# Optimization experiments

Hardware: AMD Instinct MI355X
Metric: run time of the kernel (lower is better)

Reference implementation:

```python
import jax, jax.numpy as jnp
import numpy as np

B, D, M = 16384, 512, 16

def setup_inputs() -> dict:
    key = jax.random.key(0)
    k1, k2, k3 = jax.random.split(key, 3)
    z = jax.random.normal(k1, (B, D), dtype=jnp.float32)
    # Psi: n_dynamics small [D,D] operators (orthogonal-init in torch; random here)
    Psi = jax.random.normal(k2, (M, D, D), dtype=jnp.float32) * 0.001
    gate_tokens = jax.random.normal(k3, (M, D), dtype=jnp.float32) * (1.0 / np.sqrt(D))
    t = jnp.zeros((1,), dtype=jnp.float32)  # unused by forward, kept for signature parity
    return {"t": t, "z": z, "Psi": Psi, "gate_tokens": gate_tokens}

def reference(t, z, Psi, gate_tokens):
    # scores[b,m,e] = (z @ Psi_m)[b,e]  -- batched small GEMM over M dynamics
    scores = jnp.einsum('bd,mde->bme', z, Psi)
    # gate logits and sparse-soft gates: relu(2*sigmoid(logits) - 1)
    logits = jnp.einsum('bme,me->bm', scores, gate_tokens)
    gates = jax.nn.relu(2.0 * jax.nn.sigmoid(logits) - 1.0)
    # dz[b,e] = sum_m gates[b,m] * scores[b,m,e]
    dz = jnp.einsum('bm,bme->be', gates, scores)
    return dz
```

## Files before the change

### kernel.cpp

```cpp
#include <hip/hip_runtime.h>
#include <hip/hip_bf16.h>

#define B_N 16384
#define D_N 512
#define M_N 16

typedef __attribute__((ext_vector_type(4))) float  f32x4;
typedef __attribute__((ext_vector_type(8))) short  s16x8;

__device__ __forceinline__ short bf16_of(float f) {
  union { float f; unsigned u; } v; v.f = f;
  unsigned r = v.u + 0x7fffu + ((v.u >> 16) & 1u);
  return (short)(r >> 16);
}
__device__ __forceinline__ float f32_of_bf16(unsigned short u) {
  union { unsigned u; float f; } v; v.u = ((unsigned)u) << 16; return v.f;
}
__device__ __forceinline__ void gload_lds16(const void* g, void* l) {
  __builtin_amdgcn_global_load_lds(
      (const __attribute__((address_space(1))) unsigned*)g,
      (__attribute__((address_space(3))) unsigned*)l, 16, 0, 0);
}

#define MFMA_ACC(d, x, y) d = __builtin_amdgcn_mfma_f32_16x16x32_bf16(x, y, d, 0, 0, 0)
#define MFMA_Z(d, x, y)   d = __builtin_amdgcn_mfma_f32_16x16x32_bf16(x, y, FZERO, 0, 0, 0)

__global__ void k_trw(const float* __restrict__ Psi, const float* __restrict__ gt,
                      short* __restrict__ Psib, float* __restrict__ wT) {
  int m = blockIdx.y, d0 = blockIdx.x << 6;
  __shared__ float tile[64][65];
  __shared__ float gs[D_N];
  int t = threadIdx.x;
  for (int i = t; i < D_N; i += 256) gs[i] = gt[m * D_N + i];
  int r = t >> 2, q = t & 3;
  float wacc = 0.f;
  const float* src = Psi + (size_t)m * D_N * D_N;
  short* dst = Psib + (size_t)m * D_N * D_N;
  for (int e0 = 0; e0 < D_N; e0 += 64) {
    __syncthreads();
    #pragma unroll
    for (int j = 0; j < 4; ++j) {
      int idx = t + (j << 8);
      int rr = idx >> 4, c4 = idx & 15;
      *(f32x4*)&tile[rr][c4 * 4] = *(const f32x4*)(src + (size_t)(d0 + rr) * D_N + e0 + c4 * 4);
    }
    __syncthreads();
    #pragma unroll
    for (int k = 0; k < 16; ++k) wacc += tile[r][q * 16 + k] * gs[e0 + q * 16 + k];
    #pragma unroll
    for (int it = 0; it < 2; ++it) {
      int idx = t + (it << 8);
      int el = idx >> 3, jb = idx & 7;
      int e = e0 + el;
      s16x8 o;
      #pragma unroll
      for (int k = 0; k < 8; ++k) o[k] = bf16_of(tile[jb * 8 + k][el]);
      int db = jb ^ (e & 7);
      *(s16x8*)(dst + (size_t)e * D_N + d0 + db * 8) = o;
    }
  }
  wacc += __shfl_xor(wacc, 1);
  wacc += __shfl_xor(wacc, 2);
  if (q == 0) wT[(d0 + r) * M_N + m] = wacc;
}

__global__ void k_gz(const float* __restrict__ z, const float* __restrict__ wT,
                     short* __restrict__ zb, unsigned short* __restrict__ gatesb) {
  __shared__ float zs[16][D_N];
  int t = threadIdx.x;
  size_t b0 = (size_t)blockIdx.x * 16;
  #pragma unroll
  for (int j = 0; j < 8; ++j) {
    int idx = t + (j << 8);
    int r = idx >> 7, c4 = idx & 127;
    *(f32x4*)&zs[r][c4 * 4] = *(const f32x4*)(z + (b0 + r) * D_N + c4 * 4);
  }
  __syncthreads();
  int r = t >> 4, m = t & 15;
  float s0 = 0.f, s1 = 0.f, s2 = 0.f, s3 = 0.f;
  #pragma unroll 4
  for (int e = 0; e < D_N; e += 4) {
    s0 += zs[r][e + 0] * wT[(e + 0) * M_N + m];
    s1 += zs[r][e + 1] * wT[(e + 1) * M_N + m];
    s2 += zs[r][e + 2] * wT[(e + 2) * M_N + m];
    s3 += zs[r][e + 3] * wT[(e + 3) * M_N + m];
  }
  float s = (s0 + s1) + (s2 + s3);
  float sig = 1.f / (1.f + expf(-s));
  gatesb[(b0 + r) * M_N + m] = (unsigned short)bf16_of(fmaxf(2.f * sig - 1.f, 0.f));
  #pragma unroll
  for (int j = 0; j < 4; ++j) {
    int idx = t + (j << 8);
    int rr = idx >> 6, blk = idx & 63;
    int chunk = blk >> 3, ib = blk & 7;
    int sb = ib ^ (rr & 7);
    const float* sp = &zs[rr][chunk * 64 + sb * 8];
    s16x8 o;
    #pragma unroll
    for (int k = 0; k < 8; ++k) o[k] = bf16_of(sp[k]);
    *(s16x8*)(zb + (b0 + rr) * D_N + blk * 8) = o;
  }
}

__global__ __launch_bounds__(512, 2) void k_gemm(
    const char* __restrict__ zb, const unsigned short* __restrict__ gatesb,
    const char* __restrict__ pb, float* __restrict__ dz) {
  __shared__ __align__(128) char smem[147456];
  float* glf = (float*)(smem + 131072);

  const int tid = threadIdx.x;
  const int lane = tid & 63;
  const int wid = tid >> 6;
  const int wr = wid >> 1;
  const int wc = wid & 1;
  const int bid = blockIdx.x;
  const int xcd = bid & 7;
  const int g8 = bid >> 3;
  const int bcol = g8 & 3;
  const int brow = xcd * 8 + (g8 >> 2);

  {
    s16x8 gv = *(const s16x8*)(gatesb + ((size_t)brow << 12) + ((size_t)tid << 3));
    int row = tid >> 1, mbase = (tid & 1) << 3;
    #pragma unroll
    for (int k = 0; k < 8; ++k)
      glf[(mbase + k) * 256 + row] = f32_of_bf16((unsigned short)gv[k]);
  }

  const int rsub = lane >> 3, cbyte = (lane & 7) << 4;

  auto stageA = [&](int ab, int dc) {
    #pragma unroll
    for (int j = 0; j < 4; ++j) {
      const char* g = zb + (((size_t)(brow * 256 + wid * 8 + j * 64 + rsub)) << 10)
                      + (dc << 7) + cbyte;
      gload_lds16(g, smem + ab * 32768 + (wid << 10) + (j << 13));
    }
  };
  auto stageB = [&](int s) {
    int m = s & 15, dc = s >> 4, q = s & 3;
    #pragma unroll
    for (int j = 0; j < 2; ++j) {
      const char* g = pb + (((size_t)(m * 512 + bcol * 128 + wid * 8 + j * 64 + rsub)) << 10)
                      + (dc << 7) + cbyte;
      gload_lds16(g, smem + 65536 + q * 16384 + (wid << 10) + (j << 13));
    }
  };

  const int lrow = lane & 15;
  const int swz = (lrow & 7) << 4;
  const int kq16 = (((lane >> 4) << 4)) ^ swz;
  const int offY = ((wr * 64 + lrow) << 7) + kq16;
  const int offX = ((wc * 64 + lrow) << 7) + kq16;
  const int grow = wr * 64 + lrow;

  f32x4 acc[4][4] = {};
  f32x4 accm[4][4];
  s16x8 areg[4][2];
  s16x8 bx[4], by[4];
  float gjc[4], gjn[4];
  const f32x4 FZERO = {0.f, 0.f, 0.f, 0.f};

  stageA(0, 0);
  stageB(0); stageB(1); stageB(2);
  asm volatile("s_waitcnt vmcnt(0) lgkmcnt(0)" ::: "memory");
  __builtin_amdgcn_s_barrier();
  #pragma unroll
  for (int i = 0; i < 4; ++i)
    bx[i] = *(const s16x8*)(smem + 65536 + (offX + i * 2048));
  #pragma unroll
  for (int j = 0; j < 4; ++j)
    gjc[j] = glf[grow + j * 16];

  for (int s = 0; s < 128; ++s) {
    const int m = s & 15, dc = s >> 4;
    const char* bbase_cur = smem + 65536 + (s & 3) * 16384;
    const char* bbase_nxt = smem + 65536 + ((s + 1) & 3) * 16384;

    if (m == 0) {
      const char* abase = smem + (dc & 1) * 32768;
      #pragma unroll
      for (int j = 0; j < 4; ++j) {
        areg[j][0] = *(const s16x8*)(abase + (offY + j * 2048));
        areg[j][1] = *(const s16x8*)(abase + ((offY + j * 2048) ^ 64));
      }
    }
    #pragma unroll
    for (int i = 0; i < 4; ++i)
      by[i] = *(const s16x8*)(bbase_cur + ((offX + i * 2048) ^ 64));
    {
      const int mn = (s + 1) & 15;
      #pragma unroll
      for (int j = 0; j < 4; ++j)
        gjn[j] = glf[mn * 256 + grow + j * 16];
    }
    if (s + 3 < 128) stageB(s + 3);
    if (m == 11 && dc < 7) stageA((dc & 1) ^ 1, dc + 1);

    __builtin_amdgcn_s_setprio(1);
    #pragma unroll
    for (int i = 0; i < 4; ++i)
      #pragma unroll
      for (int j = 0; j < 4; ++j)
        MFMA_Z(accm[i][j], bx[i], areg[j][0]);
    __builtin_amdgcn_s_setprio(0);

    if (s < 127) {
      #pragma unroll
      for (int i = 0; i < 4; ++i)
        bx[i] = *(const s16x8*)(bbase_nxt + (offX + i * 2048));
    }

    __builtin_amdgcn_s_setprio(1);
    #pragma unroll
    for (int i = 0; i < 4; ++i)
      #pragma unroll
      for (int j = 0; j < 4; ++j)
        MFMA_ACC(accm[i][j], by[i], areg[j][1]);
    __builtin_amdgcn_s_setprio(0);
    #pragma unroll
    for (int i = 0; i < 4; ++i)
      #pragma unroll
      for (int j = 0; j < 4; ++j)
        #pragma unroll
        for (int jj = 0; jj < 4; ++jj)
          acc[i][j][jj] = fmaf(gjc[j], accm[i][j][jj], acc[i][j][jj]);
    #pragma unroll
    for (int j = 0; j < 4; ++j) gjc[j] = gjn[j];

    if (dc < 7 && (m == 11 || m == 12))
      asm volatile("s_waitcnt vmcnt(6)" ::: "memory");
    else if (s >= 125)
      asm volatile("s_waitcnt vmcnt(0)" ::: "memory");
    else
      asm volatile("s_waitcnt vmcnt(2)" ::: "memory");
    __builtin_amdgcn_s_barrier();
  }

  #pragma unroll
  for (int i = 0; i < 4; ++i) {
    int e = bcol * 128 + wc * 64 + i * 16 + ((lane >> 4) << 2);
    #pragma unroll
    for (int j = 0; j < 4; ++j) {
      size_t b = (size_t)brow * 256 + wr * 64 + j * 16 + lrow;
      *(f32x4*)(dz + b * D_N + e) = acc[i][j];
    }
  }
}

extern "C" void kernel_launch(void* const* d_in, const int* in_sizes, int n_in,
                              void* d_out, int out_size, void* d_ws, size_t ws_size,
                              hipStream_t stream) {
  const float* z   = (const float*)d_in[1];
  const float* Psi = (const float*)d_in[2];
  const float* gt  = (const float*)d_in[3];
  float* dz = (float*)d_out;

  float* wT = (float*)d_ws;
  unsigned short* gatesb = (unsigned short*)((char*)d_ws + 32768);
  short* Psib = (short*)((char*)d_ws + 32768 + 524288);
  short* zb16 = Psib + (size_t)M_N * D_N * D_N;

  k_trw <<<dim3(8, M_N), dim3(256), 0, stream>>>(Psi, gt, Psib, wT);
  k_gz  <<<dim3(B_N / 16), dim3(256), 0, stream>>>(z, wT, zb16, gatesb);
  k_gemm<<<dim3(256), dim3(512), 0, stream>>>((const char*)zb16, gatesb,
                                              (const char*)Psib, dz);
}
```

Before: 155.1 us.

## Split Psi transpose and gate-weight reduction into two more parallel kernels

The fused transpose-and-reduce kernel ran only 128 blocks, each walking all 512 columns serially. It is replaced by two kernels: one computing wT = Psi·gate_tokens with a wave per row (512 blocks), and one doing the bf16 transpose with a 3D grid of 1024 blocks, one 64x64 tile each. This raises parallelism in the preprocessing stage, at the cost of reading Psi twice and adding an extra launch.

```diff
diff --git a/kernel.cpp b/kernel.cpp
--- a/kernel.cpp
+++ b/kernel.cpp
@@ -25,43 +25,53 @@
 #define MFMA_ACC(d, x, y) d = __builtin_amdgcn_mfma_f32_16x16x32_bf16(x, y, d, 0, 0, 0)
 #define MFMA_Z(d, x, y)   d = __builtin_amdgcn_mfma_f32_16x16x32_bf16(x, y, FZERO, 0, 0, 0)
 
-__global__ void k_trw(const float* __restrict__ Psi, const float* __restrict__ gt,
-                      short* __restrict__ Psib, float* __restrict__ wT) {
-  int m = blockIdx.y, d0 = blockIdx.x << 6;
+__global__ void k_w(const float* __restrict__ Psi, const float* __restrict__ gt,
+                    float* __restrict__ wT) {
+  int m = blockIdx.x;
+  int d0 = blockIdx.y * 16;
+  __shared__ float g[D_N];
+  for (int i = threadIdx.x; i < D_N; i += 256) g[i] = gt[m * D_N + i];
+  __syncthreads();
+  int wave = threadIdx.x >> 6, lane = threadIdx.x & 63;
+  #pragma unroll
+  for (int d = d0 + wave; d < d0 + 16; d += 4) {
+    const float* row = Psi + ((size_t)m * D_N + d) * D_N;
+    const f32x4* r4 = (const f32x4*)(row + lane * 8);
+    const f32x4* g4 = (const f32x4*)(g + lane * 8);
+    f32x4 a0 = r4[0], a1 = r4[1];
+    f32x4 b0 = g4[0], b1 = g4[1];
+    float s = a0[0]*b0[0] + a0[1]*b0[1] + a0[2]*b0[2] + a0[3]*b0[3]
+            + a1[0]*b1[0] + a1[1]*b1[1] + a1[2]*b1[2] + a1[3]*b1[3];
+    #pragma unroll
+    for (int off = 32; off; off >>= 1) s += __shfl_down(s, off);
+    if (lane == 0) wT[d * M_N + m] = s;
+  }
+}
+
+__global__ void k_tr(const float* __restrict__ Psi, short* __restrict__ Psib) {
+  int m = blockIdx.z, d0 = blockIdx.x << 6, e0 = blockIdx.y << 6;
   __shared__ float tile[64][65];
-  __shared__ float gs[D_N];
   int t = threadIdx.x;
-  for (int i = t; i < D_N; i += 256) gs[i] = gt[m * D_N + i];
-  int r = t >> 2, q = t & 3;
-  float wacc = 0.f;
   const float* src = Psi + (size_t)m * D_N * D_N;
   short* dst = Psib + (size_t)m * D_N * D_N;
-  for (int e0 = 0; e0 < D_N; e0 += 64) {
-    __syncthreads();
-    #pragma unroll
-    for (int j = 0; j < 4; ++j) {
-      int idx = t + (j << 8);
-      int rr = idx >> 4, c4 = idx & 15;
-      *(f32x4*)&tile[rr][c4 * 4] = *(const f32x4*)(src + (size_t)(d0 + rr) * D_N + e0 + c4 * 4);
-    }
-    __syncthreads();
-    #pragma unroll
-    for (int k = 0; k < 16; ++k) wacc += tile[r][q * 16 + k] * gs[e0 + q * 16 + k];
-    #pragma unroll
-    for (int it = 0; it < 2; ++it) {
-      int idx = t + (it << 8);
-      int el = idx >> 3, jb = idx & 7;
-      int e = e0 + el;
-      s16x8 o;
-      #pragma unroll
-      for (int k = 0; k < 8; ++k) o[k] = bf16_of(tile[jb * 8 + k][el]);
-      int db = jb ^ (e & 7);
-      *(s16x8*)(dst + (size_t)e * D_N + d0 + db * 8) = o;
-    }
-  }
-  wacc += __shfl_xor(wacc, 1);
-  wacc += __shfl_xor(wacc, 2);
-  if (q == 0) wT[(d0 + r) * M_N + m] = wacc;
+  #pragma unroll
+  for (int j = 0; j < 4; ++j) {
+    int idx = t + (j << 8);
+    int rr = idx >> 4, c4 = idx & 15;
+    *(f32x4*)&tile[rr][c4 * 4] = *(const f32x4*)(src + (size_t)(d0 + rr) * D_N + e0 + c4 * 4);
+  }
+  __syncthreads();
+  #pragma unroll
+  for (int it = 0; it < 2; ++it) {
+    int idx = t + (it << 8);
+    int el = idx >> 3, jb = idx & 7;
+    int e = e0 + el;
+    s16x8 o;
+    #pragma unroll
+    for (int k = 0; k < 8; ++k) o[k] = bf16_of(tile[jb * 8 + k][el]);
+    int db = jb ^ (e & 7);
+    *(s16x8*)(dst + (size_t)e * D_N + d0 + db * 8) = o;
+  }
 }
 
 __global__ void k_gz(const float* __restrict__ z, const float* __restrict__ wT,
@@ -261,8 +271,9 @@
   short* Psib = (short*)((char*)d_ws + 32768 + 524288);
   short* zb16 = Psib + (size_t)M_N * D_N * D_N;
 
-  k_trw <<<dim3(8, M_N), dim3(256), 0, stream>>>(Psi, gt, Psib, wT);
-  k_gz  <<<dim3(B_N / 16), dim3(256), 0, stream>>>(z, wT, zb16, gatesb);
-  k_gemm<<<dim3(256), dim3(512), 0, stream>>>((const char*)zb16, gatesb,
-                                              (const char*)Psib, dz);
-}
+  k_w   <<<dim3(M_N, 32),   dim3(256), 0, stream>>>(Psi, gt, wT);
+  k_tr  <<<dim3(8, 8, M_N), dim3(256), 0, stream>>>(Psi, Psib);
+  k_gz  <<<dim3(B_N / 16),  dim3(256), 0, stream>>>(z, wT, zb16, gatesb);
+  k_gemm<<<dim3(256),       dim3(512), 0, stream>>>((const char*)zb16, gatesb,
+                                                    (const char*)Psib, dz);
+}
```

Result: no change. 153.8 us (median of 2 runs) (-0.8%).
